# Optimization experiments

Hardware: AMD Instinct MI355X
Metric: run time of the kernel (lower is better)

Reference implementation:

```python
import jax, jax.numpy as jnp
import numpy as np

B, T, N = 2, 512, 512
H = 64          # hidden_dim
S = 8           # static_dim
C = 8           # coord_dim
DYN = 4         # dynamic feature dim (hard-coded in module)
SELF_LOOP_W = 1.0


def setup_inputs() -> dict:
    key = jax.random.key(0)
    ks = jax.random.split(key, 12)
    x = jax.random.normal(ks[0], (B, T, N), dtype=jnp.float32)
    mask = jax.random.randint(ks[1], (B, T, N), 0, 2).astype(jnp.float32)
    static_context = jax.random.normal(ks[2], (N, S), dtype=jnp.float32)
    node_coords = jax.random.normal(ks[3], (N, C), dtype=jnp.float32)
    sc = 0.1
    W1 = jax.random.normal(ks[4], (DYN + S, H), dtype=jnp.float32) * sc
    b1 = jnp.zeros((H,), dtype=jnp.float32)
    W2 = jax.random.normal(ks[5], (H, H), dtype=jnp.float32) * sc
    b2 = jnp.zeros((H,), dtype=jnp.float32)
    W3 = jax.random.normal(ks[6], (4 * H, H), dtype=jnp.float32) * sc
    b3 = jnp.zeros((H,), dtype=jnp.float32)
    W4 = jax.random.normal(ks[7], (H, 1), dtype=jnp.float32) * sc
    b4 = jnp.zeros((1,), dtype=jnp.float32)
    return {"x": x, "mask": mask, "static_context": static_context,
            "node_coords": node_coords, "W1": W1, "b1": b1, "W2": W2,
            "b2": b2, "W3": W3, "b3": b3, "W4": W4, "b4": b4}


def _dynamic_context(x, mask):
    observed = 1.0 - mask                                  # (B,T,N)
    count = jnp.maximum(observed.sum(axis=1), 1.0)          # (B,N)
    mean = (x * observed).sum(axis=1) / count               # (B,N)
    centered = (x - mean[:, None, :]) * observed
    std = jnp.sqrt((centered ** 2).sum(axis=1) / count + 1e-6)
    # last observed value per node
    t_idx = jnp.arange(x.shape[1], dtype=x.dtype)[None, :, None]
    latest = jnp.argmax(t_idx * observed, axis=1)           # (B,N) int
    last = jnp.take_along_axis(x, latest[:, None, :], axis=1)[:, 0, :]
    missing_ratio = mask.mean(axis=1)                       # (B,N)
    return jnp.stack([mean, std, last, missing_ratio], axis=-1)  # (B,N,4)


def _prior_adjacency(node_coords):
    diff = node_coords[:, None, :] - node_coords[None, :, :]  # (N,N,C)
    d2 = (diff ** 2).sum(-1)
    dist = jnp.where(d2 > 0, jnp.sqrt(jnp.where(d2 > 0, d2, 1.0)), 0.0)
    prior = 1.0 / (1.0 + dist)
    eye = jnp.eye(node_coords.shape[0], dtype=node_coords.dtype)
    return prior * (1.0 - eye)


def reference(x, mask, static_context, node_coords, W1, b1, W2, b2, W3, b3, W4, b4):
    batch = x.shape[0]
    node_dynamic = _dynamic_context(x, mask)                         # (B,N,4)
    node_static = jnp.broadcast_to(static_context[None], (batch,) + static_context.shape)
    feats = jnp.concatenate([node_dynamic, node_static], axis=-1)    # (B,N,4+S)
    h = jax.nn.relu(feats @ W1 + b1)
    node_repr = jax.nn.relu(h @ W2 + b2)                              # (B,N,H)

    h_i = node_repr[:, :, None, :]                                    # (B,N,1,H)
    h_j = node_repr[:, None, :, :]                                    # (B,1,N,H)
    hi = jnp.broadcast_to(h_i, (batch, N, N, H))
    hj = jnp.broadcast_to(h_j, (batch, N, N, H))
    pair = jnp.concatenate([hi, hj, jnp.abs(hi - hj), hi * hj], axis=-1)  # (B,N,N,4H)
    e = jax.nn.relu(pair @ W3 + b3)
    edge_mod = jax.nn.relu((e @ W4 + b4)[..., 0])                     # (B,N,N)

    prior = _prior_adjacency(node_coords)[None]                       # (1,N,N)
    eye = jnp.eye(N, dtype=x.dtype)[None]
    adapt = edge_mod * prior + eye * SELF_LOOP_W
    degree = jnp.maximum(adapt.sum(axis=-1), 1e-6)                    # (B,N)
    inv_sqrt = degree ** -0.5
    return inv_sqrt[:, :, None] * adapt * inv_sqrt[:, None, :]
```

## Files before the change

kernel.cpp:

```cpp
#include <hip/hip_runtime.h>
#include <math.h>

#define B_ 2
#define T_ 512
#define N_ 512
#define H_ 64

typedef _Float16 half8 __attribute__((ext_vector_type(8)));
typedef __attribute__((ext_vector_type(4))) float floatx4;

__device__ inline half8 habs8(half8 v) {
    union { half8 h; unsigned u[4]; } x; x.h = v;
    x.u[0] &= 0x7fff7fffu; x.u[1] &= 0x7fff7fffu;
    x.u[2] &= 0x7fff7fffu; x.u[3] &= 0x7fff7fffu;
    return x.h;
}

__global__ void prep_kernel(const float* __restrict__ x, const float* __restrict__ mask,
                            const float* __restrict__ coords, const float* __restrict__ W3,
                            float* __restrict__ part, float* __restrict__ prior,
                            _Float16* __restrict__ W3ph) {
    int blk = blockIdx.x;
    if (blk < 512) {
        int b  = blk >> 8;
        int nc = (blk >> 5) & 7;
        int tc = blk & 31;
        int tn = threadIdx.x & 63;
        int tt = threadIdx.x >> 6;
        int n  = nc * 64 + tn;

        float sx = 0.f, sxx = 0.f, cnt = 0.f, msum = 0.f, bv = 0.f, bt = -1.f;
#pragma unroll
        for (int it = 0; it < 4; it++) {
            int t = tc * 16 + it * 4 + tt;
            int off = (b * T_ + t) * N_ + n;
            float xv = x[off];
            float mv = mask[off];
            float obs = 1.f - mv;
            sx   += xv * obs;
            sxx  += xv * xv * obs;
            cnt  += obs;
            msum += mv;
            if (obs > 0.5f) { bt = (float)t; bv = xv; }
        }

        __shared__ float red[6][4][64];
        red[0][tt][tn] = sx;  red[1][tt][tn] = sxx; red[2][tt][tn] = cnt;
        red[3][tt][tn] = msum; red[4][tt][tn] = bv; red[5][tt][tn] = bt;
        __syncthreads();

        if (threadIdx.x < 64) {
            float Sx = 0.f, Sxx = 0.f, Cnt = 0.f, Ms = 0.f, Bv = 0.f, Bt = -1.f;
#pragma unroll
            for (int u = 0; u < 4; u++) {
                Sx  += red[0][u][tn];
                Sxx += red[1][u][tn];
                Cnt += red[2][u][tn];
                Ms  += red[3][u][tn];
                float btu = red[5][u][tn];
                if (btu > Bt) { Bt = btu; Bv = red[4][u][tn]; }
            }
            const int plane = B_ * 32 * N_;
            int base = (b * 32 + tc) * N_ + n;
            part[0 * plane + base] = Sx;
            part[1 * plane + base] = Sxx;
            part[2 * plane + base] = Cnt;
            part[3 * plane + base] = Ms;
            part[4 * plane + base] = Bv;
            part[5 * plane + base] = Bt;
        }
    } else if (blk < 1536) {
        int idx = (blk - 512) * 256 + threadIdx.x;
        int i = idx >> 9, j = idx & (N_ - 1);
        float d2 = 0.f;
#pragma unroll
        for (int c = 0; c < 8; c++) {
            float df = coords[i * 8 + c] - coords[j * 8 + c];
            d2 += df * df;
        }
        float dist = (d2 > 0.f) ? sqrtf(d2) : 0.f;
        prior[idx] = (i == j) ? 0.f : 1.f / (1.f + dist);
    } else {
        int k = (blk - 1536) * 256 + threadIdx.x;
        int t = k & 7;
        int l = (k >> 3) & 63;
        int f = k >> 9;
        int s = f >> 2, nt = f & 3;
        int quad = l >> 4, col = l & 15;
        W3ph[k] = (_Float16)W3[(128 + s * 32 + quad * 8 + t) * H_ + nt * 16 + col];
    }
}

__global__ __launch_bounds__(64) void node_kernel(
        const float* __restrict__ part, const float* __restrict__ x,
        const float* __restrict__ sc,
        const float* __restrict__ W1, const float* __restrict__ b1,
        const float* __restrict__ W2, const float* __restrict__ b2,
        const float* __restrict__ W3,
        _Float16* __restrict__ nrh, float* __restrict__ P, float* __restrict__ Qp) {
    int blk = blockIdx.x;
    int b = blk >> 9;
    int n = blk & (N_ - 1);
    int o = threadIdx.x;

    __shared__ float f[12];
    __shared__ float h[H_];
    __shared__ float r[H_];

    {
        const int plane = B_ * 32 * N_;
        float Sx = 0.f, Sxx = 0.f, Cnt = 0.f, Ms = 0.f, Bv = 0.f, Bt = -1.f;
        if (o < 32) {
            int base = (b * 32 + o) * N_ + n;
            Sx  = part[0 * plane + base];
            Sxx = part[1 * plane + base];
            Cnt = part[2 * plane + base];
            Ms  = part[3 * plane + base];
            Bv  = part[4 * plane + base];
            Bt  = part[5 * plane + base];
        }
#pragma unroll
        for (int off = 1; off < 32; off <<= 1) {
            Sx  += __shfl_xor(Sx, off);
            Sxx += __shfl_xor(Sxx, off);
            Cnt += __shfl_xor(Cnt, off);
            Ms  += __shfl_xor(Ms, off);
            float obt = __shfl_xor(Bt, off);
            float obv = __shfl_xor(Bv, off);
            if (obt > Bt) { Bt = obt; Bv = obv; }
        }
        if (o == 0) {
            float count = fmaxf(Cnt, 1.f);
            float mean  = Sx / count;
            float var   = (Sxx - 2.f * mean * Sx + mean * mean * Cnt) / count;
            float stdv  = sqrtf(fmaxf(var, 0.f) + 1e-6f);
            float last  = (Bt >= 0.f) ? Bv : x[b * T_ * N_ + n];
            f[0] = mean; f[1] = stdv; f[2] = last; f[3] = Ms * (1.f / (float)T_);
        }
        if (o >= 4 && o < 12) f[o] = sc[n * 8 + (o - 4)];
    }
    __syncthreads();

    float a = b1[o];
#pragma unroll
    for (int k = 0; k < 12; k++) a += f[k] * W1[k * H_ + o];
    h[o] = fmaxf(a, 0.f);
    __syncthreads();

    float a2 = b2[o];
#pragma unroll 8
    for (int k = 0; k < H_; k++) a2 += h[k] * W2[k * H_ + o];
    float rv = fmaxf(a2, 0.f);
    r[o] = rv;
    nrh[(b * N_ + n) * H_ + o] = (_Float16)rv;
    __syncthreads();

    float p = 0.f, q = 0.f;
#pragma unroll 8
    for (int k = 0; k < H_; k++) {
        float rk = r[k];
        p += rk * W3[k * H_ + o];
        q += rk * W3[(H_ + k) * H_ + o];
    }
    P[(b * N_ + n) * H_ + o] = p;
    Qp[(b * N_ + n) * H_ + (o & 15) * 4 + (o >> 4)] = q;
}

__global__ __launch_bounds__(256) void pair_mfma_kernel(
        const _Float16* __restrict__ nrh, const float* __restrict__ P,
        const float* __restrict__ Qp, const _Float16* __restrict__ W3ph,
        const float* __restrict__ b3, const float* __restrict__ W4,
        const float* __restrict__ b4, const float* __restrict__ prior,
        float* __restrict__ adapt, float* __restrict__ degree) {
    int blk = blockIdx.x;
    int rb = blk >> 9;
    int i = blk & (N_ - 1);
    int tid = threadIdx.x;
    int w = tid >> 6;
    int l = tid & 63;
    int col = l & 15;
    int quad = l >> 4;

    half8 bf[4][4];
#pragma unroll
    for (int s = 0; s < 4; s++)
#pragma unroll
        for (int nt = 0; nt < 4; nt++)
            bf[s][nt] = *(const half8*)(W3ph + (((s * 4 + nt) * 64 + l) << 3));

    const _Float16* hi_row = nrh + (rb * N_ + i) * H_;
    half8 hiA = *(const half8*)(hi_row + quad * 8);
    half8 hiB = *(const half8*)(hi_row + 32 + quad * 8);

    float pb3[4], w4v[4];
#pragma unroll
    for (int nt = 0; nt < 4; nt++) {
        int o = nt * 16 + col;
        pb3[nt] = P[(rb * N_ + i) * H_ + o] + b3[o];
        w4v[nt] = W4[o];
    }
    float b4s = b4[0];
    const float* prow = prior + i * N_;
    const _Float16* nrb = nrh + (rb * N_) * H_;
    float rsum = 0.f;

    half8 hA, hB;
    {
        const _Float16* p0 = nrb + (w * 128 + col) * H_;
        hA = *(const half8*)(p0 + quad * 8);
        hB = *(const half8*)(p0 + 32 + quad * 8);
    }

#pragma unroll
    for (int mt = 0; mt < 8; mt++) {
        int j0 = w * 128 + mt * 16;

        half8 nA, nB;
        if (mt < 7) {
            const _Float16* pn = nrb + (j0 + 16 + col) * H_;
            nA = *(const half8*)(pn + quad * 8);
            nB = *(const half8*)(pn + 32 + quad * 8);
        }

        floatx4 pv = *(const floatx4*)(prow + j0 + quad * 4);
        floatx4 qv[4];
#pragma unroll
        for (int r = 0; r < 4; r++)
            qv[r] = *(const floatx4*)(Qp + (rb * N_ + j0 + quad * 4 + r) * H_ + col * 4);

        half8 dA = habs8(hiA - hA);
        half8 dB = habs8(hiB - hB);
        half8 mA = hiA * hA;
        half8 mB = hiB * hB;

        floatx4 acc[4];
#pragma unroll
        for (int nt = 0; nt < 4; nt++) acc[nt] = (floatx4){0.f, 0.f, 0.f, 0.f};
#pragma unroll
        for (int nt = 0; nt < 4; nt++) {
            acc[nt] = __builtin_amdgcn_mfma_f32_16x16x32_f16(dA, bf[0][nt], acc[nt], 0, 0, 0);
            acc[nt] = __builtin_amdgcn_mfma_f32_16x16x32_f16(dB, bf[1][nt], acc[nt], 0, 0, 0);
            acc[nt] = __builtin_amdgcn_mfma_f32_16x16x32_f16(mA, bf[2][nt], acc[nt], 0, 0, 0);
            acc[nt] = __builtin_amdgcn_mfma_f32_16x16x32_f16(mB, bf[3][nt], acc[nt], 0, 0, 0);
        }

        float ed[4];
#pragma unroll
        for (int r = 0; r < 4; r++) {
            int j = j0 + quad * 4 + r;
            float p = 0.f;
#pragma unroll
            for (int nt = 0; nt < 4; nt++)
                p += fmaxf(acc[nt][r] + pb3[nt] + qv[r][nt], 0.f) * w4v[nt];
            p += __shfl_xor(p, 1);
            p += __shfl_xor(p, 2);
            p += __shfl_xor(p, 4);
            p += __shfl_xor(p, 8);
            float edge = fmaxf(p + b4s, 0.f);
            float ad = (j == i) ? 1.0f : edge * pv[r];
            ed[r] = ad;
            rsum += ad;
        }
        if (col == 0) {
            *(floatx4*)&adapt[(size_t)(rb * N_ + i) * N_ + j0 + quad * 4] =
                (floatx4){ed[0], ed[1], ed[2], ed[3]};
        }
        if (mt < 7) { hA = nA; hB = nB; }
    }

    rsum += __shfl_xor(rsum, 16);
    rsum += __shfl_xor(rsum, 32);
    __shared__ float sRow[4];
    if (l == 0) sRow[w] = rsum;
    __syncthreads();
    if (tid == 0) degree[rb * N_ + i] = sRow[0] + sRow[1] + sRow[2] + sRow[3];
}

__global__ void norm_kernel(const float* __restrict__ adapt, const float* __restrict__ deg,
                            float* __restrict__ out) {
    int idx = blockIdx.x * 256 + threadIdx.x;
    int b = idx >> 16;
    int r = (idx >> 7) & (N_ - 1);
    int c4 = (idx & 127) << 2;
    float dr = rsqrtf(fmaxf(deg[b * N_ + r], 1e-6f));
    floatx4 a = *(const floatx4*)(adapt + ((size_t)idx << 2));
    floatx4 o;
#pragma unroll
    for (int k = 0; k < 4; k++)
        o[k] = dr * a[k] * rsqrtf(fmaxf(deg[b * N_ + c4 + k], 1e-6f));
    *(floatx4*)(out + ((size_t)idx << 2)) = o;
}

extern "C" void kernel_launch(void* const* d_in, const int* in_sizes, int n_in,
                              void* d_out, int out_size, void* d_ws, size_t ws_size,
                              hipStream_t stream) {
    const float* x      = (const float*)d_in[0];
    const float* mask   = (const float*)d_in[1];
    const float* sc     = (const float*)d_in[2];
    const float* coords = (const float*)d_in[3];
    const float* W1 = (const float*)d_in[4];
    const float* b1 = (const float*)d_in[5];
    const float* W2 = (const float*)d_in[6];
    const float* b2 = (const float*)d_in[7];
    const float* W3 = (const float*)d_in[8];
    const float* b3 = (const float*)d_in[9];
    const float* W4 = (const float*)d_in[10];
    const float* b4 = (const float*)d_in[11];
    float* out = (float*)d_out;

    float* wsp = (float*)d_ws;
    float* P       = wsp;
    float* Qp      = wsp + 65536;
    float* prior   = wsp + 131072;
    _Float16* nrh  = (_Float16*)(wsp + 393216);
    _Float16* W3ph = (_Float16*)(wsp + 425984);
    float* deg     = wsp + 430080;
    float* adapt   = wsp + 431104;
    float* part    = adapt;

    prep_kernel<<<1568, 256, 0, stream>>>(x, mask, coords, W3, part, prior, W3ph);
    node_kernel<<<B_ * N_, 64, 0, stream>>>(part, x, sc, W1, b1, W2, b2, W3, nrh, P, Qp);
    pair_mfma_kernel<<<B_ * N_, 256, 0, stream>>>(nrh, P, Qp, W3ph, b3, W4, b4, prior, adapt, deg);
    norm_kernel<<<512, 256, 0, stream>>>(adapt, deg, out);
}
```

Baseline: 113.3 us.

## Fuse prep and node kernels into one launch with wave-level reductions

```diff
diff --git a/kernel.cpp b/kernel.cpp
--- a/kernel.cpp
+++ b/kernel.cpp
@@ -16,23 +16,25 @@
     return x.h;
 }
 
-__global__ void prep_kernel(const float* __restrict__ x, const float* __restrict__ mask,
-                            const float* __restrict__ coords, const float* __restrict__ W3,
-                            float* __restrict__ part, float* __restrict__ prior,
-                            _Float16* __restrict__ W3ph) {
+__global__ __launch_bounds__(64) void node_kernel(
+        const float* __restrict__ x, const float* __restrict__ mask,
+        const float* __restrict__ sc, const float* __restrict__ coords,
+        const float* __restrict__ W1, const float* __restrict__ b1,
+        const float* __restrict__ W2, const float* __restrict__ b2,
+        const float* __restrict__ W3,
+        _Float16* __restrict__ nrh, float* __restrict__ P, float* __restrict__ Qp,
+        float* __restrict__ prior, _Float16* __restrict__ W3ph) {
     int blk = blockIdx.x;
-    if (blk < 512) {
-        int b  = blk >> 8;
-        int nc = (blk >> 5) & 7;
-        int tc = blk & 31;
-        int tn = threadIdx.x & 63;
-        int tt = threadIdx.x >> 6;
-        int n  = nc * 64 + tn;
+    int o = threadIdx.x;
+
+    if (blk < 1024) {
+        int b = blk >> 9;
+        int n = blk & (N_ - 1);
 
         float sx = 0.f, sxx = 0.f, cnt = 0.f, msum = 0.f, bv = 0.f, bt = -1.f;
 #pragma unroll
-        for (int it = 0; it < 4; it++) {
-            int t = tc * 16 + it * 4 + tt;
+        for (int k = 0; k < 8; k++) {
+            int t = o + (k << 6);
             int off = (b * T_ + t) * N_ + n;
             float xv = x[off];
             float mv = mask[off];
@@ -43,45 +45,69 @@
             msum += mv;
             if (obs > 0.5f) { bt = (float)t; bv = xv; }
         }
-
-        __shared__ float red[6][4][64];
-        red[0][tt][tn] = sx;  red[1][tt][tn] = sxx; red[2][tt][tn] = cnt;
-        red[3][tt][tn] = msum; red[4][tt][tn] = bv; red[5][tt][tn] = bt;
-        __syncthreads();
-
-        if (threadIdx.x < 64) {
-            float Sx = 0.f, Sxx = 0.f, Cnt = 0.f, Ms = 0.f, Bv = 0.f, Bt = -1.f;
-#pragma unroll
-            for (int u = 0; u < 4; u++) {
-                Sx  += red[0][u][tn];
-                Sxx += red[1][u][tn];
-                Cnt += red[2][u][tn];
-                Ms  += red[3][u][tn];
-                float btu = red[5][u][tn];
-                if (btu > Bt) { Bt = btu; Bv = red[4][u][tn]; }
+#pragma unroll
+        for (int off = 1; off < 64; off <<= 1) {
+            sx   += __shfl_xor(sx, off);
+            sxx  += __shfl_xor(sxx, off);
+            cnt  += __shfl_xor(cnt, off);
+            msum += __shfl_xor(msum, off);
+            float obt = __shfl_xor(bt, off);
+            float obv = __shfl_xor(bv, off);
+            if (obt > bt) { bt = obt; bv = obv; }
+        }
+        float count = fmaxf(cnt, 1.f);
+        float mean  = sx / count;
+        float var   = (sxx - 2.f * mean * sx + mean * mean * cnt) / count;
+        float stdv  = sqrtf(fmaxf(var, 0.f) + 1e-6f);
+        float last  = (bt >= 0.f) ? bv : x[b * T_ * N_ + n];
+        float mr    = msum * (1.f / (float)T_);
+
+        float a = b1[o] + mean * W1[o] + stdv * W1[H_ + o] +
+                  last * W1[2 * H_ + o] + mr * W1[3 * H_ + o];
+#pragma unroll
+        for (int c = 0; c < 8; c++)
+            a += sc[n * 8 + c] * W1[(4 + c) * H_ + o];
+        float h = fmaxf(a, 0.f);
+
+        float a2 = b2[o];
+#pragma unroll 16
+        for (int k = 0; k < H_; k++)
+            a2 += __shfl(h, k) * W2[k * H_ + o];
+        float rv = fmaxf(a2, 0.f);
+        nrh[(b * N_ + n) * H_ + o] = (_Float16)rv;
+
+        float p = 0.f, q = 0.f;
+#pragma unroll 16
+        for (int k = 0; k < H_; k++) {
+            float rk = __shfl(rv, k);
+            p += rk * W3[k * H_ + o];
+            q += rk * W3[(H_ + k) * H_ + o];
+        }
+        P[(b * N_ + n) * H_ + o] = p;
+        Qp[(b * N_ + n) * H_ + (o & 15) * 4 + (o >> 4)] = q;
+    } else if (blk < 2048) {
+        int e = (blk - 1024) * 256 + o * 4;
+        int pi = e >> 9;
+        int pj = e & (N_ - 1);
+        float ci[8];
+#pragma unroll
+        for (int c = 0; c < 8; c++) ci[c] = coords[pi * 8 + c];
+        floatx4 pr;
+#pragma unroll
+        for (int r = 0; r < 4; r++) {
+            int j = pj + r;
+            float d2 = 0.f;
+#pragma unroll
+            for (int c = 0; c < 8; c++) {
+                float df = ci[c] - coords[j * 8 + c];
+                d2 += df * df;
             }
-            const int plane = B_ * 32 * N_;
-            int base = (b * 32 + tc) * N_ + n;
-            part[0 * plane + base] = Sx;
-            part[1 * plane + base] = Sxx;
-            part[2 * plane + base] = Cnt;
-            part[3 * plane + base] = Ms;
-            part[4 * plane + base] = Bv;
-            part[5 * plane + base] = Bt;
-        }
-    } else if (blk < 1536) {
-        int idx = (blk - 512) * 256 + threadIdx.x;
-        int i = idx >> 9, j = idx & (N_ - 1);
-        float d2 = 0.f;
-#pragma unroll
-        for (int c = 0; c < 8; c++) {
-            float df = coords[i * 8 + c] - coords[j * 8 + c];
-            d2 += df * df;
-        }
-        float dist = (d2 > 0.f) ? sqrtf(d2) : 0.f;
-        prior[idx] = (i == j) ? 0.f : 1.f / (1.f + dist);
+            float dist = (d2 > 0.f) ? sqrtf(d2) : 0.f;
+            pr[r] = (pi == j) ? 0.f : 1.f / (1.f + dist);
+        }
+        *(floatx4*)(prior + e) = pr;
     } else {
-        int k = (blk - 1536) * 256 + threadIdx.x;
+        int k = (blk - 2048) * 64 + o;
         int t = k & 7;
         int l = (k >> 3) & 63;
         int f = k >> 9;
@@ -89,81 +115,6 @@
         int quad = l >> 4, col = l & 15;
         W3ph[k] = (_Float16)W3[(128 + s * 32 + quad * 8 + t) * H_ + nt * 16 + col];
     }
-}
-
-__global__ __launch_bounds__(64) void node_kernel(
-        const float* __restrict__ part, const float* __restrict__ x,
-        const float* __restrict__ sc,
-        const float* __restrict__ W1, const float* __restrict__ b1,
-        const float* __restrict__ W2, const float* __restrict__ b2,
-        const float* __restrict__ W3,
-        _Float16* __restrict__ nrh, float* __restrict__ P, float* __restrict__ Qp) {
-    int blk = blockIdx.x;
-    int b = blk >> 9;
-    int n = blk & (N_ - 1);
-    int o = threadIdx.x;
-
-    __shared__ float f[12];
-    __shared__ float h[H_];
-    __shared__ float r[H_];
-
-    {
-        const int plane = B_ * 32 * N_;
-        float Sx = 0.f, Sxx = 0.f, Cnt = 0.f, Ms = 0.f, Bv = 0.f, Bt = -1.f;
-        if (o < 32) {
-            int base = (b * 32 + o) * N_ + n;
-            Sx  = part[0 * plane + base];
-            Sxx = part[1 * plane + base];
-            Cnt = part[2 * plane + base];
-            Ms  = part[3 * plane + base];
-            Bv  = part[4 * plane + base];
-            Bt  = part[5 * plane + base];
-        }
-#pragma unroll
-        for (int off = 1; off < 32; off <<= 1) {
-            Sx  += __shfl_xor(Sx, off);
-            Sxx += __shfl_xor(Sxx, off);
-            Cnt += __shfl_xor(Cnt, off);
-            Ms  += __shfl_xor(Ms, off);
-            float obt = __shfl_xor(Bt, off);
-            float obv = __shfl_xor(Bv, off);
-            if (obt > Bt) { Bt = obt; Bv = obv; }
-        }
-        if (o == 0) {
-            float count = fmaxf(Cnt, 1.f);
-            float mean  = Sx / count;
-            float var   = (Sxx - 2.f * mean * Sx + mean * mean * Cnt) / count;
-            float stdv  = sqrtf(fmaxf(var, 0.f) + 1e-6f);
-            float last  = (Bt >= 0.f) ? Bv : x[b * T_ * N_ + n];
-            f[0] = mean; f[1] = stdv; f[2] = last; f[3] = Ms * (1.f / (float)T_);
-        }
-        if (o >= 4 && o < 12) f[o] = sc[n * 8 + (o - 4)];
-    }
-    __syncthreads();
-
-    float a = b1[o];
-#pragma unroll
-    for (int k = 0; k < 12; k++) a += f[k] * W1[k * H_ + o];
-    h[o] = fmaxf(a, 0.f);
-    __syncthreads();
-
-    float a2 = b2[o];
-#pragma unroll 8
-    for (int k = 0; k < H_; k++) a2 += h[k] * W2[k * H_ + o];
-    float rv = fmaxf(a2, 0.f);
-    r[o] = rv;
-    nrh[(b * N_ + n) * H_ + o] = (_Float16)rv;
-    __syncthreads();
-
-    float p = 0.f, q = 0.f;
-#pragma unroll 8
-    for (int k = 0; k < H_; k++) {
-        float rk = r[k];
-        p += rk * W3[k * H_ + o];
-        q += rk * W3[(H_ + k) * H_ + o];
-    }
-    P[(b * N_ + n) * H_ + o] = p;
-    Qp[(b * N_ + n) * H_ + (o & 15) * 4 + (o >> 4)] = q;
 }
 
 __global__ __launch_bounds__(256) void pair_mfma_kernel(
@@ -316,10 +267,9 @@
     _Float16* W3ph = (_Float16*)(wsp + 425984);
     float* deg     = wsp + 430080;
     float* adapt   = wsp + 431104;
-    float* part    = adapt;
-
-    prep_kernel<<<1568, 256, 0, stream>>>(x, mask, coords, W3, part, prior, W3ph);
-    node_kernel<<<B_ * N_, 64, 0, stream>>>(part, x, sc, W1, b1, W2, b2, W3, nrh, P, Qp);
+
+    node_kernel<<<2176, 64, 0, stream>>>(x, mask, sc, coords, W1, b1, W2, b2, W3,
+                                         nrh, P, Qp, prior, W3ph);
     pair_mfma_kernel<<<B_ * N_, 256, 0, stream>>>(nrh, P, Qp, W3ph, b3, W4, b4, prior, adapt, deg);
     norm_kernel<<<512, 256, 0, stream>>>(adapt, deg, out);
 }
```

Measured after the change: 113.8 us. Within noise of the previous version (+0.5%).
